# Optimization experiments

Hardware: AMD Instinct MI355X
Metric: run time of the kernel (lower is better)

Reference implementation:

```python
import jax, jax.numpy as jnp
import numpy as np

K = 3          # kernel_size per pseudo-coordinate dim
DIM = 3        # edge_attr dimensionality
M = K ** DIM   # total number of spline kernel weight matrices


def spline_conv(x, src, dst, pseudo, W, Wr, b):
    """Degree-1 open B-spline conv (torch_geometric SplineConv, aggr='mean').
    x: (N, C_in), pseudo: (E, DIM) in [0,1], W: (M, C_in, C_out), Wr: (C_in, C_out), b: (C_out,).
    """
    N, C_in = x.shape
    pos = pseudo * (K - 1)                      # (E, DIM) in [0, K-1]
    i0 = jnp.clip(jnp.floor(pos), 0, K - 2)     # lower knot index per dim
    frac = pos - i0                             # (E, DIM) linear basis fraction
    i0 = i0.astype(jnp.int32)
    strides = jnp.array([1, K, K * K], dtype=jnp.int32)
    xj = x[src]                                 # (E, C_in) irregular gather
    # accumulate basis-weighted neighbor features per (dst node, kernel index)
    acc = jnp.zeros((N * M, C_in), dtype=x.dtype)
    for bits in range(2 ** DIM):                # 8 corners of the linear B-spline support
        off = jnp.array([(bits >> d) & 1 for d in range(DIM)], dtype=jnp.int32)
        w = jnp.prod(jnp.where(off == 1, frac, 1.0 - frac), axis=1)       # (E,)
        kidx = jnp.sum((i0 + off[None, :]) * strides[None, :], axis=1)    # (E,) flat kernel idx
        acc = acc.at[dst * M + kidx].add(w[:, None] * xj)                 # scatter-add
    out = jnp.einsum('nmi,mio->no', acc.reshape(N, M, C_in), W)
    deg = jnp.zeros((N,), x.dtype).at[dst].add(1.0)                        # in-degree
    out = out / jnp.maximum(deg, 1.0)[:, None]                             # mean aggregation
    return out + x @ Wr + b                                                # root weight + bias


def setup_inputs() -> dict:
    key = jax.random.key(0)
    ks = jax.random.split(key, 16)
    N, E = 50000, 800000
    dims = [3, 64, 64, 64]
    inp = {
        "x": jax.random.normal(ks[0], (N, 3), jnp.float32),
        "edge_index": jax.random.randint(ks[1], (2, E), 0, N),
        "edge_attr": jax.random.uniform(ks[2], (E, DIM), dtype=jnp.float32),
    }
    for l in range(3):
        ci, co = dims[l], dims[l + 1]
        inp[f"W{l}"] = jax.random.normal(ks[3 + 3 * l], (M, ci, co), jnp.float32) * (1.0 / np.sqrt(ci * M))
        inp[f"root{l}"] = jax.random.normal(ks[4 + 3 * l], (ci, co), jnp.float32) * (1.0 / np.sqrt(ci))
        inp[f"b{l}"] = jnp.zeros((co,), jnp.float32)
    return inp


def reference(x, edge_index, edge_attr, W0, root0, b0, W1, root1, b1, W2, root2, b2):
    src, dst = edge_index[0], edge_index[1]   # PyG flow: source_to_target
    h = x
    for W, Wr, b in ((W0, root0, b0), (W1, root1, b1), (W2, root2, b2)):
        h = jax.nn.relu(spline_conv(h, src, dst, edge_attr, W, Wr, b))
    return h
```

## Files before the change

kernel.cpp:

```cpp
#include <hip/hip_runtime.h>
#include <cstdint>


typedef __attribute__((ext_vector_type(8))) short short8;
typedef __attribute__((ext_vector_type(4))) float floatx4;

#define AS1 __attribute__((address_space(1)))
#define AS3 __attribute__((address_space(3)))

__device__ inline short f2bf(float f) {
    union { float f; unsigned u; } x; x.f = f;
    unsigned r = x.u + 0x7FFF + ((x.u >> 16) & 1);
    return (short)(r >> 16);
}

__device__ inline float bf2f(unsigned short u) {
    union { unsigned u; float f; } x;
    x.u = ((unsigned)u) << 16;
    return x.f;
}


__global__ void count_kernel(const int* __restrict__ ei, int* __restrict__ count, int E) {
    int e = blockIdx.x * blockDim.x + threadIdx.x;
    if (e < E) atomicAdd(&count[ei[E + e]], 1);
}

__global__ __launch_bounds__(1024) void scan_tile_kernel(const int* __restrict__ count,
                                                         int* __restrict__ row_ptr,
                                                         int* __restrict__ bsum, int N) {
    __shared__ int wsum[16];
    int tid = threadIdx.x, lane = tid & 63, wid = tid >> 6;
    int i = blockIdx.x * 1024 + tid;
    int v = (i < N) ? count[i] : 0;
    int incl = v;
#pragma unroll
    for (int off = 1; off < 64; off <<= 1) {
        int t = __shfl_up(incl, off, 64);
        if (lane >= off) incl += t;
    }
    if (lane == 63) wsum[wid] = incl;
    __syncthreads();
    if (tid < 16) {
        int w = wsum[tid];
#pragma unroll
        for (int off = 1; off < 16; off <<= 1) {
            int t = __shfl_up(w, off, 16);
            if ((tid & 15) >= off) w += t;
        }
        wsum[tid] = w;
    }
    __syncthreads();
    int waveoff = (wid > 0) ? wsum[wid - 1] : 0;
    if (i < N) row_ptr[i] = waveoff + incl - v;
    if (tid == 1023) bsum[blockIdx.x] = waveoff + incl;
}

__global__ __launch_bounds__(64) void scan_bsum_kernel(const int* __restrict__ bsum,
                                                       int* __restrict__ boff,
                                                       int* __restrict__ tot, int nb) {
    int tid = threadIdx.x;
    int v = (tid < nb) ? bsum[tid] : 0;
    int incl = v;
#pragma unroll
    for (int off = 1; off < 64; off <<= 1) {
        int t = __shfl_up(incl, off, 64);
        if (tid >= off) incl += t;
    }
    boff[tid] = incl - v;
    if (tid == 63) tot[0] = incl;
}

__global__ __launch_bounds__(1024) void scan_add_kernel(int* __restrict__ row_ptr,
                                                        const int* __restrict__ boff,
                                                        const int* __restrict__ tot,
                                                        int* __restrict__ cursor, int N) {
    int i = blockIdx.x * 1024 + threadIdx.x;
    if (i < N) {
        int r = row_ptr[i] + boff[blockIdx.x];
        row_ptr[i] = r;
        cursor[i] = r;
    }
    if (i == 0) row_ptr[N] = tot[0];
}

__global__ void basis_sort_kernel(const int* __restrict__ ei, const float* __restrict__ attr,
                                  const int* __restrict__ count, int* __restrict__ cursor,
                                  unsigned short* __restrict__ s_wcol, int E) {
    int e = blockIdx.x * blockDim.x + threadIdx.x;
    if (e >= E) return;
    int src = ei[e];
    int dst = ei[E + e];
    float f[3]; int i0[3];
#pragma unroll
    for (int d = 0; d < 3; d++) {
        float pos = attr[e * 3 + d] * 2.0f;
        float fl = floorf(pos);
        fl = fminf(fmaxf(fl, 0.0f), 1.0f);
        i0[d] = (int)fl;
        f[d] = pos - fl;
    }
    int base = i0[0] + 3 * i0[1] + 9 * i0[2];
    float invd = 1.0f / fmaxf((float)count[dst], 1.0f);
    int p = atomicAdd(&cursor[dst], 1);
    float w[8];
#pragma unroll
    for (int c = 0; c < 8; c++) {
        float ww = invd;
#pragma unroll
        for (int d = 0; d < 3; d++) {
            int off = (c >> d) & 1;
            ww *= off ? f[d] : (1.0f - f[d]);
        }
        w[c] = ww;
    }
    unsigned short* wc = s_wcol + (size_t)p * 32;
    short8 z8 = {0, 0, 0, 0, 0, 0, 0, 0};
    *(short8*)(wc) = z8;
    *(short8*)(wc + 8) = z8;
    *(short8*)(wc + 16) = z8;
    *(short8*)(wc + 24) = z8;
#pragma unroll
    for (int c = 0; c < 8; c++) {
        int coff = (c & 1) + 3 * ((c >> 1) & 1) + 9 * (c >> 2);
        wc[base + coff] = (unsigned short)f2bf(w[c]);
    }
    wc[27] = (unsigned short)(src & 0xFFFF);
    wc[28] = (unsigned short)((src >> 16) | (base << 8));
}

__global__ void build_wb2(const float* __restrict__ Wa, const float* __restrict__ Ra,
                          unsigned short* __restrict__ wba,
                          const float* __restrict__ Wb, const float* __restrict__ Rb,
                          unsigned short* __restrict__ wbb) {
    int idx0 = blockIdx.x * blockDim.x + threadIdx.x;
    int half = idx0 / (4 * 56 * 64);
    if (half >= 2) return;
    int idx = idx0 - half * (4 * 56 * 64);
    const float* W = half ? Wb : Wa;
    const float* Wr = half ? Rb : Ra;
    unsigned short* wb = half ? wbb : wba;
    int l = idx & 63;
    int c = (idx >> 6) % 56;
    int t = idx / (56 * 64);
    int q = l >> 4, o = t * 16 + (l & 15);
    short8 out;
#pragma unroll
    for (int j = 0; j < 8; j++) {
        int k = c * 32 + q * 8 + j;
        float v = (k < 1728) ? W[(size_t)k * 64 + o] : Wr[(size_t)(k - 1728) * 64 + o];
        out[j] = f2bf(v);
    }
    *(short8*)(wb + (size_t)idx * 8) = out;
}

__global__ __launch_bounds__(256) void layer0_kernel(
    const float* __restrict__ x, const float* __restrict__ W0,
    const float* __restrict__ Wr, const float* __restrict__ bias,
    const int* __restrict__ row_ptr,
    const unsigned short* __restrict__ s_wcol, unsigned short* __restrict__ h_out, int N) {
    constexpr int NPB = 16, KT = 84;
    __shared__ __align__(16) float acc[NPB * 2 * KT];
    int tid = threadIdx.x, lane = tid & 63, wv = tid >> 6;
    int n0 = blockIdx.x * NPB;
    for (int k = tid; k < NPB * 2 * KT; k += 256) acc[k] = 0.0f;
    __syncthreads();

    int d = lane >> 5, hl = lane & 31;
    int c = hl / 3, i = hl - c * 3;
    bool act = (hl < 24);
    int cc = act ? c : 0;
    int coff = (cc & 1) + 3 * ((cc >> 1) & 1) + 9 * (cc >> 2);

    for (int g2 = 0; g2 < 4; g2++) {
        int g = wv * 4 + g2;
        int n = n0 + g;
        if (n >= N) continue;
        if (lane < 3) acc[(g * 2) * KT + 81 + lane] = x[(size_t)n * 3 + lane];
        int rs = row_ptr[n], re = row_ptr[n + 1];
        int npairs = (re - rs + 1) >> 1;
        float* accd = &acc[(g * 2 + d) * KT];
        for (int pb = 0; pb < npairs; pb += 8) {
            int srcs[8], kidxs[8]; float ws_[8], xs_[8];
#pragma unroll
            for (int j = 0; j < 8; j++) {
                int ej = rs + (pb + j) * 2 + d;
                bool v = (pb + j < npairs) && (ej < re);
                int ec = v ? ej : rs;
                const unsigned short* wc = s_wcol + (size_t)ec * 32;
                int m27 = wc[27], m28 = wc[28];
                srcs[j] = m27 | ((m28 & 0xFF) << 16);
                int base = (m28 >> 8) & 0xF;
                kidxs[j] = base + coff;
                float wv_ = bf2f(wc[base + coff]);
                ws_[j] = v ? wv_ : 0.0f;
            }
#pragma unroll
            for (int j = 0; j < 8; j++)
                xs_[j] = x[(size_t)srcs[j] * 3 + i];
#pragma unroll
            for (int j = 0; j < 8; j++) {
                if (act) accd[kidxs[j] * 3 + i] += ws_[j] * xs_[j];
            }
        }
    }
    __syncthreads();

    int o = lane;
    float wreg[KT];
#pragma unroll
    for (int k = 0; k < KT; k++)
        wreg[k] = (k < 81) ? W0[k * 64 + o] : Wr[(k - 81) * 64 + o];
    float bv = bias[o];
    for (int g = wv; g < NPB; g += 4) {
        int n = n0 + g;
        if (n >= N) break;
        float s = bv;
#pragma unroll
        for (int k4 = 0; k4 < KT; k4 += 4) {
            floatx4 a0 = *(const floatx4*)&acc[(g * 2) * KT + k4];
            floatx4 a1 = *(const floatx4*)&acc[(g * 2 + 1) * KT + k4];
            s += (a0.x + a1.x) * wreg[k4] + (a0.y + a1.y) * wreg[k4 + 1]
               + (a0.z + a1.z) * wreg[k4 + 2] + (a0.w + a1.w) * wreg[k4 + 3];
        }
        h_out[(size_t)n * 64 + o] = (unsigned short)f2bf(fmaxf(s, 0.0f));
    }
}

template <bool OUTF32>
__global__ __launch_bounds__(512, 4) void layer64_kernel(
    const unsigned short* __restrict__ h_in, const unsigned short* __restrict__ wb,
    const float* __restrict__ bias, const int* __restrict__ row_ptr,
    const unsigned short* __restrict__ s_wcol,
    const unsigned short* __restrict__ zpad, void* __restrict__ h_out, int N) {
    constexpr int NPB = 8;
    constexpr int RGS = 3088;
    __shared__ __align__(16) unsigned short lds[NPB * RGS];
    int tid = threadIdx.x, lane = tid & 63;
    int wvu = __builtin_amdgcn_readfirstlane(tid >> 6);
    int n0 = blockIdx.x * NPB;
    int srow = lane & 15, sgrp = lane >> 4;

    unsigned short* reg = &lds[(size_t)wvu * RGS];
    unsigned short* featL = reg;
    unsigned short* wcolL = reg + 2048;

#define STAGE_WCOL(CB) do { \
    _Pragma("unroll") for (int k = 0; k < 2; k++) { \
        int el = (CB) + k * 16 + (lane >> 2); \
        const unsigned short* srcp = (el < dw) \
            ? s_wcol + (size_t)(rs + wbo + el) * 32 + (lane & 3) * 8 \
            : zpad + (lane & 3) * 8; \
        __builtin_amdgcn_global_load_lds((const AS1 unsigned int*)srcp, \
            (AS3 unsigned int*)(wcolL + k * 512), 16, 0, 0); \
    } \
} while (0)

    {
        int n = n0 + wvu;
        if (n >= N) {
            for (int k = lane; k < 1792; k += 64) reg[k] = 0;
        } else {
            {
                short8 z = {0, 0, 0, 0, 0, 0, 0, 0};
#pragma unroll
                for (int s = 0; s < 4; s++)
                    *(short8*)(featL + lane * 8 + s * 512) = z;
            }
            floatx4 facc[2][4];
#pragma unroll
            for (int mt = 0; mt < 2; mt++)
#pragma unroll
                for (int nt = 0; nt < 4; nt++)
                    facc[mt][nt] = (floatx4){0.0f, 0.0f, 0.0f, 0.0f};

            int rs = row_ptr[n], re = row_ptr[n + 1];
            int deg = re - rs;
            for (int wbo = 0; wbo < deg; wbo += 64) {
                int dw = deg - wbo;
                STAGE_WCOL(0);
                asm volatile("s_waitcnt vmcnt(0)" ::: "memory");
                int vmax = (dw < 64 ? dw : 64) - 1;
                for (int ch2 = 0; ch2 < 2; ch2++) {
                    int cb = ch2 * 32;
                    if (cb >= dw) break;
                    int nsl = dw - cb; if (nsl > 32) nsl = 32;
                    int ngl = (nsl + 7) >> 3;
                    for (int i = 0; i < ngl; i++) {
                        int elc = i * 8 + (lane >> 3);
                        if (cb + elc > vmax) elc = vmax - cb;
                        const unsigned short* wrc = wcolL + elc * 32;
                        int ms = wrc[27] | ((wrc[28] & 0xFF) << 16);
                        int c3 = (lane & 7) ^ (i << 1);
                        const unsigned short* srcp = h_in + (size_t)ms * 64 + c3 * 8;
                        __builtin_amdgcn_global_load_lds(
                            (const AS1 unsigned int*)srcp,
                            (AS3 unsigned int*)(featL + i * 512), 16, 0, 0);
                    }
                    short8 af0, af1;
                    {
                        const unsigned short* wrp = wcolL + (8 * sgrp) * 32 + srow;
#pragma unroll
                        for (int j = 0; j < 8; j++) {
                            af0[j] = (short)wrp[j * 32];
                            af1[j] = (short)wrp[j * 32 + 16];
                        }
                    }
                    if (ch2 == 0 && dw > 32) {
                        asm volatile("s_waitcnt lgkmcnt(0)" ::: "memory");
                        __builtin_amdgcn_sched_barrier(0);
                        STAGE_WCOL(32);
                    }
                    asm volatile("s_waitcnt vmcnt(0)" ::: "memory");
#pragma unroll
                    for (int nt = 0; nt < 4; nt++) {
                        short8 bn;
#pragma unroll
                        for (int jj = 0; jj < 8; jj++) {
                            int e = sgrp * 8 + jj;
                            int g = e * 8 + (((nt * 2) + (srow >> 3)) ^ (sgrp << 1));
                            bn[jj] = (short)featL[g * 8 + (srow & 7)];
                        }
                        facc[0][nt] = __builtin_amdgcn_mfma_f32_16x16x32_bf16(
                            af0, bn, facc[0][nt], 0, 0, 0);
                        facc[1][nt] = __builtin_amdgcn_mfma_f32_16x16x32_bf16(
                            af1, bn, facc[1][nt], 0, 0, 0);
                    }
                }
            }
#pragma unroll
            for (int mt = 0; mt < 2; mt++)
#pragma unroll
                for (int nt = 0; nt < 4; nt++)
#pragma unroll
                    for (int r = 0; r < 4; r++) {
                        int mrow = mt * 16 + sgrp * 4 + r;
                        if (mrow < 27)
                            reg[mrow * 64 + nt * 16 + srow] =
                                (unsigned short)f2bf(facc[mt][nt][r]);
                    }
            reg[1728 + lane] = h_in[(size_t)n * 64 + lane];
        }
    }
#undef STAGE_WCOL
    __syncthreads();

    {
        floatx4 f0 = {0.0f, 0.0f, 0.0f, 0.0f};
        floatx4 f1 = {0.0f, 0.0f, 0.0f, 0.0f};
        if (wvu < 4) {
            int hf = wvu >> 1;
            int tp = wvu & 1;
            const unsigned short* ap = lds + (size_t)(lane & 7) * RGS + ((lane >> 4) * 8);
            const unsigned short* wbp0 = wb + ((size_t)((tp * 2) * 56) * 64 + lane) * 8;
            const unsigned short* wbp1 = wb + ((size_t)((tp * 2 + 1) * 56) * 64 + lane) * 8;
#pragma unroll
            for (int ci = 0; ci < 28; ci++) {
                int c = hf * 28 + ci;
                short8 af = *(const short8*)(ap + c * 32);
                short8 b0 = *(const short8*)(wbp0 + (size_t)c * 64 * 8);
                short8 b1 = *(const short8*)(wbp1 + (size_t)c * 64 * 8);
                f0 = __builtin_amdgcn_mfma_f32_16x16x32_bf16(af, b0, f0, 0, 0, 0);
                f1 = __builtin_amdgcn_mfma_f32_16x16x32_bf16(af, b1, f1, 0, 0, 0);
            }
        }
        __syncthreads();
        if (wvu < 4) {
            float* pfw = (float*)(lds + (size_t)wvu * RGS);
#pragma unroll
            for (int r = 0; r < 4; r++) {
                pfw[r * 64 + lane] = f0[r];
                pfw[256 + r * 64 + lane] = f1[r];
            }
        }
        __syncthreads();
        if (wvu < 4) {
            int t = wvu;
            int o = t * 16 + (lane & 15);
            float bv = bias[o];
            const float* pfA = (const float*)(lds + (size_t)(t >> 1) * RGS)
                             + (t & 1) * 256;
            const float* pfB = (const float*)(lds + (size_t)(2 + (t >> 1)) * RGS)
                             + (t & 1) * 256;
#pragma unroll
            for (int r = 0; r < 4; r++) {
                int m = (lane >> 4) * 4 + r;
                if (m < 8) {
                    int n = n0 + m;
                    if (n < N) {
                        float s = pfA[r * 64 + lane] + pfB[r * 64 + lane];
                        float val = fmaxf(s + bv, 0.0f);
                        if (OUTF32) {
                            ((float*)h_out)[(size_t)n * 64 + o] = val;
                        } else {
                            ((unsigned short*)h_out)[(size_t)n * 64 + o] =
                                (unsigned short)f2bf(val);
                        }
                    }
                }
            }
        }
    }
}

extern "C" void kernel_launch(void* const* d_in, const int* in_sizes, int n_in,
                              void* d_out, int out_size, void* d_ws, size_t ws_size,
                              hipStream_t stream) {
    (void)n_in; (void)out_size; (void)ws_size;
    const float* x    = (const float*)d_in[0];
    const int*   ei   = (const int*)d_in[1];
    const float* attr = (const float*)d_in[2];
    const float* W0 = (const float*)d_in[3];
    const float* R0 = (const float*)d_in[4];
    const float* B0 = (const float*)d_in[5];
    const float* W1 = (const float*)d_in[6];
    const float* R1 = (const float*)d_in[7];
    const float* B1 = (const float*)d_in[8];
    const float* W2 = (const float*)d_in[9];
    const float* R2 = (const float*)d_in[10];
    const float* B2 = (const float*)d_in[11];
    const int N = in_sizes[0] / 3;
    const int E = in_sizes[1] / 2;

    char* ws = (char*)d_ws;
    size_t off = 0;
    auto alloc = [&](size_t bytes) {
        size_t cur = off;
        off = (off + bytes + 255) & ~(size_t)255;
        return cur;
    };
    int* row_ptr = (int*)(ws + alloc((size_t)(N + 1) * 4));
    int* count   = (int*)(ws + alloc((size_t)N * 4));
    int* cursor  = (int*)(ws + alloc((size_t)N * 4));
    int* bsum    = (int*)(ws + alloc(64 * 4));
    int* boff    = (int*)(ws + alloc(64 * 4));
    int* tot     = (int*)(ws + alloc(4));
    unsigned short* zpad = (unsigned short*)(ws + alloc(256));
    unsigned short* s_wcol = (unsigned short*)(ws + alloc((size_t)E * 32 * 2));
    unsigned short* h_a  = (unsigned short*)(ws + alloc((size_t)N * 64 * 2));
    unsigned short* h_b  = (unsigned short*)(ws + alloc((size_t)N * 64 * 2));
    unsigned short* wb1  = (unsigned short*)(ws + alloc((size_t)4 * 56 * 64 * 8 * 2));
    unsigned short* wb2  = (unsigned short*)(ws + alloc((size_t)4 * 56 * 64 * 8 * 2));

    int nb = (N + 1023) / 1024;

    hipMemsetAsync(count, 0, (size_t)N * 4, stream);
    hipMemsetAsync(zpad, 0, 256, stream);
    count_kernel<<<(E + 255) / 256, 256, 0, stream>>>(ei, count, E);
    scan_tile_kernel<<<nb, 1024, 0, stream>>>(count, row_ptr, bsum, N);
    scan_bsum_kernel<<<1, 64, 0, stream>>>(bsum, boff, tot, nb);
    scan_add_kernel<<<nb, 1024, 0, stream>>>(row_ptr, boff, tot, cursor, N);
    basis_sort_kernel<<<(E + 255) / 256, 256, 0, stream>>>(ei, attr, count, cursor,
                                                           s_wcol, E);
    build_wb2<<<(2 * 4 * 56 * 64 + 255) / 256, 256, 0, stream>>>(W1, R1, wb1,
                                                                 W2, R2, wb2);

    layer0_kernel<<<(N + 15) / 16, 256, 0, stream>>>(x, W0, R0, B0, row_ptr,
                                                     s_wcol, h_a, N);
    layer64_kernel<false><<<(N + 7) / 8, 512, 0, stream>>>(h_a, wb1, B1, row_ptr,
                                                           s_wcol, zpad, h_b, N);
    layer64_kernel<true><<<(N + 7) / 8, 512, 0, stream>>>(h_b, wb2, B2, row_ptr,
                                                          s_wcol, zpad, d_out, N);
}
```

Before: 386.7 us.

## Fuse layer-0 aggregation into the basis-sort kernel using global atomics

The first-layer neighbour aggregation moves into the edge-basis kernel: each edge atomically adds its eight basis-weighted source features into a per-node 84-float global buffer. The layer-0 kernel then only reads that buffer and applies W0, the root weight and the bias. This removes the separate CSR gather pass over edges for layer 0. In exchange it adds 24 scattered float atomics per edge, a 16.8 MB memset and an extra read of the accumulator, and the summation order is no longer deterministic.

```diff
diff --git a/kernel.cpp b/kernel.cpp
--- a/kernel.cpp
+++ b/kernel.cpp
@@ -85,8 +85,10 @@
 }
 
 __global__ void basis_sort_kernel(const int* __restrict__ ei, const float* __restrict__ attr,
+                                  const float* __restrict__ x,
                                   const int* __restrict__ count, int* __restrict__ cursor,
-                                  unsigned short* __restrict__ s_wcol, int E) {
+                                  unsigned short* __restrict__ s_wcol,
+                                  float* __restrict__ acc84, int E) {
     int e = blockIdx.x * blockDim.x + threadIdx.x;
     if (e >= E) return;
     int src = ei[e];
@@ -127,6 +129,18 @@
     }
     wc[27] = (unsigned short)(src & 0xFFFF);
     wc[28] = (unsigned short)((src >> 16) | (base << 8));
+    float x0 = x[(size_t)src * 3];
+    float x1 = x[(size_t)src * 3 + 1];
+    float x2 = x[(size_t)src * 3 + 2];
+    float* ad = acc84 + (size_t)dst * 84;
+#pragma unroll
+    for (int c = 0; c < 8; c++) {
+        int coff = (c & 1) + 3 * ((c >> 1) & 1) + 9 * (c >> 2);
+        int kb = (base + coff) * 3;
+        atomicAdd(&ad[kb], w[c] * x0);
+        atomicAdd(&ad[kb + 1], w[c] * x1);
+        atomicAdd(&ad[kb + 2], w[c] * x2);
+    }
 }
 
 __global__ void build_wb2(const float* __restrict__ Wa, const float* __restrict__ Ra,
@@ -154,75 +168,32 @@
     *(short8*)(wb + (size_t)idx * 8) = out;
 }
 
-__global__ __launch_bounds__(256) void layer0_kernel(
-    const float* __restrict__ x, const float* __restrict__ W0,
-    const float* __restrict__ Wr, const float* __restrict__ bias,
-    const int* __restrict__ row_ptr,
-    const unsigned short* __restrict__ s_wcol, unsigned short* __restrict__ h_out, int N) {
-    constexpr int NPB = 16, KT = 84;
-    __shared__ __align__(16) float acc[NPB * 2 * KT];
+__global__ __launch_bounds__(256) void layer0b_kernel(
+    const float* __restrict__ x, const float* __restrict__ acc84,
+    const float* __restrict__ W0, const float* __restrict__ Wr,
+    const float* __restrict__ bias, unsigned short* __restrict__ h_out, int N) {
+    constexpr int NPB = 64;
     int tid = threadIdx.x, lane = tid & 63, wv = tid >> 6;
     int n0 = blockIdx.x * NPB;
-    for (int k = tid; k < NPB * 2 * KT; k += 256) acc[k] = 0.0f;
-    __syncthreads();
-
-    int d = lane >> 5, hl = lane & 31;
-    int c = hl / 3, i = hl - c * 3;
-    bool act = (hl < 24);
-    int cc = act ? c : 0;
-    int coff = (cc & 1) + 3 * ((cc >> 1) & 1) + 9 * (cc >> 2);
-
-    for (int g2 = 0; g2 < 4; g2++) {
-        int g = wv * 4 + g2;
-        int n = n0 + g;
-        if (n >= N) continue;
-        if (lane < 3) acc[(g * 2) * KT + 81 + lane] = x[(size_t)n * 3 + lane];
-        int rs = row_ptr[n], re = row_ptr[n + 1];
-        int npairs = (re - rs + 1) >> 1;
-        float* accd = &acc[(g * 2 + d) * KT];
-        for (int pb = 0; pb < npairs; pb += 8) {
-            int srcs[8], kidxs[8]; float ws_[8], xs_[8];
-#pragma unroll
-            for (int j = 0; j < 8; j++) {
-                int ej = rs + (pb + j) * 2 + d;
-                bool v = (pb + j < npairs) && (ej < re);
-                int ec = v ? ej : rs;
-                const unsigned short* wc = s_wcol + (size_t)ec * 32;
-                int m27 = wc[27], m28 = wc[28];
-                srcs[j] = m27 | ((m28 & 0xFF) << 16);
-                int base = (m28 >> 8) & 0xF;
-                kidxs[j] = base + coff;
-                float wv_ = bf2f(wc[base + coff]);
-                ws_[j] = v ? wv_ : 0.0f;
-            }
-#pragma unroll
-            for (int j = 0; j < 8; j++)
-                xs_[j] = x[(size_t)srcs[j] * 3 + i];
-#pragma unroll
-            for (int j = 0; j < 8; j++) {
-                if (act) accd[kidxs[j] * 3 + i] += ws_[j] * xs_[j];
-            }
-        }
-    }
-    __syncthreads();
-
     int o = lane;
-    float wreg[KT];
-#pragma unroll
-    for (int k = 0; k < KT; k++)
+    float wreg[84];
+#pragma unroll
+    for (int k = 0; k < 84; k++)
         wreg[k] = (k < 81) ? W0[k * 64 + o] : Wr[(k - 81) * 64 + o];
     float bv = bias[o];
     for (int g = wv; g < NPB; g += 4) {
         int n = n0 + g;
         if (n >= N) break;
+        const float* ap = acc84 + (size_t)n * 84;
         float s = bv;
 #pragma unroll
-        for (int k4 = 0; k4 < KT; k4 += 4) {
-            floatx4 a0 = *(const floatx4*)&acc[(g * 2) * KT + k4];
-            floatx4 a1 = *(const floatx4*)&acc[(g * 2 + 1) * KT + k4];
-            s += (a0.x + a1.x) * wreg[k4] + (a0.y + a1.y) * wreg[k4 + 1]
-               + (a0.z + a1.z) * wreg[k4 + 2] + (a0.w + a1.w) * wreg[k4 + 3];
-        }
+        for (int k4 = 0; k4 < 84; k4 += 4) {
+            floatx4 a = *(const floatx4*)&ap[k4];
+            s += a.x * wreg[k4] + a.y * wreg[k4 + 1]
+               + a.z * wreg[k4 + 2] + a.w * wreg[k4 + 3];
+        }
+        s += x[(size_t)n * 3] * wreg[81] + x[(size_t)n * 3 + 1] * wreg[82]
+           + x[(size_t)n * 3 + 2] * wreg[83];
         h_out[(size_t)n * 64 + o] = (unsigned short)f2bf(fmaxf(s, 0.0f));
     }
 }
@@ -437,6 +408,7 @@
     int* tot     = (int*)(ws + alloc(4));
     unsigned short* zpad = (unsigned short*)(ws + alloc(256));
     unsigned short* s_wcol = (unsigned short*)(ws + alloc((size_t)E * 32 * 2));
+    float* acc84 = (float*)(ws + alloc((size_t)N * 84 * 4));
     unsigned short* h_a  = (unsigned short*)(ws + alloc((size_t)N * 64 * 2));
     unsigned short* h_b  = (unsigned short*)(ws + alloc((size_t)N * 64 * 2));
     unsigned short* wb1  = (unsigned short*)(ws + alloc((size_t)4 * 56 * 64 * 8 * 2));
@@ -446,17 +418,17 @@
 
     hipMemsetAsync(count, 0, (size_t)N * 4, stream);
     hipMemsetAsync(zpad, 0, 256, stream);
+    hipMemsetAsync(acc84, 0, (size_t)N * 84 * 4, stream);
     count_kernel<<<(E + 255) / 256, 256, 0, stream>>>(ei, count, E);
     scan_tile_kernel<<<nb, 1024, 0, stream>>>(count, row_ptr, bsum, N);
     scan_bsum_kernel<<<1, 64, 0, stream>>>(bsum, boff, tot, nb);
     scan_add_kernel<<<nb, 1024, 0, stream>>>(row_ptr, boff, tot, cursor, N);
-    basis_sort_kernel<<<(E + 255) / 256, 256, 0, stream>>>(ei, attr, count, cursor,
-                                                           s_wcol, E);
+    basis_sort_kernel<<<(E + 255) / 256, 256, 0, stream>>>(ei, attr, x, count, cursor,
+                                                           s_wcol, acc84, E);
     build_wb2<<<(2 * 4 * 56 * 64 + 255) / 256, 256, 0, stream>>>(W1, R1, wb1,
                                                                  W2, R2, wb2);
 
-    layer0_kernel<<<(N + 15) / 16, 256, 0, stream>>>(x, W0, R0, B0, row_ptr,
-                                                     s_wcol, h_a, N);
+    layer0b_kernel<<<(N + 63) / 64, 256, 0, stream>>>(x, acc84, W0, R0, B0, h_a, N);
     layer64_kernel<false><<<(N + 7) / 8, 512, 0, stream>>>(h_a, wb1, B1, row_ptr,
                                                            s_wcol, zpad, h_b, N);
     layer64_kernel<true><<<(N + 7) / 8, 512, 0, stream>>>(h_b, wb2, B2, row_ptr,
```

New measurement: 1.381 ms. 257% more time.
